# Kernel tuning notes

Measured on AMD Instinct MI355X. Metric: run time of the kernel, lower is better.

## Reference

```python
import jax, jax.numpy as jnp
import numpy as np

B, C, H, W, G = 4, 256, 64, 64, 4
K = 9  # 3x3 kernel


def _conv1x1(x, w, b):
    return jnp.einsum('bchw,oc->bohw', x, w) + b[None, :, None, None]


def _deform_conv(V, offset, mask, weight, groups):
    # torchvision modulated deform_conv2d, stride=1, pad=1, dil=1, no bias.
    Bs, Cc, Hh, Ww = V.shape
    Cg = Cc // groups
    # offset layout: [B, og, K, 2(y,x), H, W]
    off = offset.reshape(Bs, groups, K, 2, Hh, Ww)
    ky, kx = jnp.meshgrid(jnp.arange(3), jnp.arange(3), indexing='ij')
    ky = ky.reshape(K).astype(offset.dtype)
    kx = kx.reshape(K).astype(offset.dtype)
    hh = jnp.arange(Hh, dtype=offset.dtype)
    ww = jnp.arange(Ww, dtype=offset.dtype)
    # sampling positions [B, G, K, H, W]
    py = off[:, :, :, 0] + (hh[:, None] - 1.0)[None, None, None] + ky[None, None, :, None, None]
    px = off[:, :, :, 1] + (ww[None, :] - 1.0)[None, None, None] + kx[None, None, :, None, None]
    y0f = jnp.floor(py)
    x0f = jnp.floor(px)
    fy = py - y0f
    fx = px - x0f
    y0 = y0f.astype(jnp.int32)
    x0 = x0f.astype(jnp.int32)
    Vg = V.reshape(Bs, groups, Cg, Hh * Ww)

    def gather(yi, xi, wgt):
        valid = (yi >= 0) & (yi < Hh) & (xi >= 0) & (xi < Ww)
        idx = (jnp.clip(yi, 0, Hh - 1) * Ww + jnp.clip(xi, 0, Ww - 1)).reshape(Bs, groups, 1, K * Hh * Ww)
        vals = jnp.take_along_axis(Vg, jnp.broadcast_to(idx, (Bs, groups, Cg, K * Hh * Ww)), axis=3)
        vals = vals.reshape(Bs, groups, Cg, K, Hh, Ww)
        return vals * (wgt * valid.astype(wgt.dtype))[:, :, None]

    sampled = (gather(y0, x0, (1.0 - fy) * (1.0 - fx))
               + gather(y0, x0 + 1, (1.0 - fy) * fx)
               + gather(y0 + 1, x0, fy * (1.0 - fx))
               + gather(y0 + 1, x0 + 1, fy * fx))  # [B, G, Cg, K, H, W]
    m = mask.reshape(Bs, groups, K, Hh, Ww)
    wk = weight.reshape(groups, Cc // groups, Cg, K)
    out = jnp.einsum('bgikhw,bgkhw,goik->bgohw', sampled, m, wk)
    return out.reshape(Bs, Cc, Hh, Ww)


def setup_inputs() -> dict:
    key = jax.random.key(0)
    ks = jax.random.split(key, 12)
    inp = {
        'rife_feat': jax.random.normal(ks[0], (B, C, H, W), jnp.float32),
        'd0': jax.random.normal(ks[1], (B, C, H, W), jnp.float32),
        'd1': jax.random.normal(ks[2], (B, C, H, W), jnp.float32),
        'wq': jax.random.normal(ks[3], (C, C), jnp.float32) * (1.0 / np.sqrt(C)),
        'bq': jax.random.normal(ks[4], (C,), jnp.float32) * 0.01,
        'wk': jax.random.normal(ks[5], (C, C), jnp.float32) * (1.0 / np.sqrt(C)),
        'bk': jax.random.normal(ks[6], (C,), jnp.float32) * 0.01,
        'wv': jax.random.normal(ks[7], (C, C), jnp.float32) * (1.0 / np.sqrt(C)),
        'bv': jax.random.normal(ks[8], (C,), jnp.float32) * 0.01,
        'w_off': jax.random.normal(ks[9], (27 * G, 2 * C, 3, 3), jnp.float32) * 0.02,
        'b_off': jnp.zeros((27 * G,), jnp.float32),
        'dcn_w': jax.random.normal(ks[10], (C, C // G, 3, 3), jnp.float32) * 0.05,
        'gamma': jnp.ones((1,), jnp.float32),
    }
    return inp


def reference(rife_feat, d0, d1, wq, bq, wk, bk, wv, bv, w_off, b_off, dcn_w, gamma):
    Qs = jnp.concatenate([rife_feat, rife_feat], axis=0)  # [2B, C, H, W]
    Ds = jnp.concatenate([d0, d1], axis=0)
    Q = _conv1x1(Qs, wq, bq)
    Kf = _conv1x1(Ds, wk, bk)
    V = _conv1x1(Ds, wv, bv)
    comb = jnp.concatenate([Q, Kf], axis=1)  # [2B, 2C, H, W]
    out = jax.lax.conv_general_dilated(comb, w_off, (1, 1), [(1, 1), (1, 1)],
                                       dimension_numbers=('NCHW', 'OIHW', 'NCHW'))
    out = out + b_off[None, :, None, None]  # [2B, 27G, H, W]
    n = out.shape[1] // 3
    o1, o2, mlog = out[:, :n], out[:, n:2 * n], out[:, 2 * n:]
    offset = jnp.concatenate([o1, o2], axis=1)  # [2B, 18G, H, W]
    mask = jax.nn.sigmoid(mlog)
    aligned = _deform_conv(V, offset, mask, dcn_w, G)
    a0, a1 = aligned[:B], aligned[B:]
    fused = rife_feat + gamma * (a0 + a1)
    return fused, offset[:B], offset[B:]
```

## Files before the change

kernel.cpp:

```cpp
#include <hip/hip_runtime.h>
#include <math.h>

#define HW   4096
#define CDIM 256

typedef float f32x4  __attribute__((ext_vector_type(4)));
typedef float f32x2  __attribute__((ext_vector_type(2)));
typedef short short8 __attribute__((ext_vector_type(8)));

#define FUSED_SZ (4ULL*256*HW)
#define OFF_SZ   (4ULL*72*HW)

static __device__ __forceinline__ unsigned short f2b(float f) {
    unsigned u = __float_as_uint(f);
    unsigned r = (u + 0x7fffu + ((u >> 16) & 1u)) >> 16;
    return (unsigned short)r;
}
static __device__ __forceinline__ float b2f(short h) {
    return __uint_as_float(((unsigned)(unsigned short)h) << 16);
}
static __device__ __forceinline__ unsigned pk_bf16(float a, float b) {
    unsigned r;
    asm("v_cvt_pk_bf16_f32 %0, %1, %2" : "=v"(r) : "v"(a), "v"(b));
    return r;
}
union U8 { unsigned u[4]; short8 s; };

#define CVT8(a, HI) ((f32x2)__builtin_amdgcn_cvt_pk_f32_fp8((int)(a), HI))

__global__ __launch_bounds__(256) void prep_all(
    const float* __restrict__ w_off, const float* __restrict__ dcn_w,
    const float* __restrict__ wq, const float* __restrict__ wk,
    const float* __restrict__ wv,
    unsigned short* __restrict__ wT2, unsigned short* __restrict__ dcnwT,
    unsigned short* __restrict__ wqkvT)
{
    const int bid = blockIdx.x;
    if (bid < 2304) {
        int idx = bid * 256 + threadIdx.x;
        int kk  = idx / (128 * 512);
        int rem = idx - kk * 128 * 512;
        int o = rem >> 9;
        int c = rem & 511;
        float v = (o < 108) ? w_off[((size_t)o * 512 + c) * 9 + kk] : 0.f;
        size_t flat = ((size_t)(kk * 16 + (c >> 5)) * 128 + o) * 32 + (c & 31);
        wT2[flat] = f2b(v);
    } else if (bid < 2880) {
        int idx = (bid - 2304) * 256 + threadIdx.x;
        if (idx < 9 * 256 * 64) {
            int k   = idx / (256 * 64);
            int rem = idx - k * 256 * 64;
            int og = rem >> 6;
            int i  = rem & 63;
            int g = og >> 6, ol = og & 63;
            size_t flat = ((size_t)((k * 4 + g) * 2 + (i >> 5)) * 64 + ol) * 32 + (i & 31);
            dcnwT[flat] = f2b(dcn_w[((size_t)og * 64 + i) * 9 + k]);
        }
    } else {
        int idx = (bid - 2880) * 256 + threadIdx.x;
        int o = idx >> 8;
        int c = idx & 255;
        float v = (o < 256) ? wq[(size_t)o * 256 + c]
                : (o < 512) ? wk[(size_t)(o - 256) * 256 + c]
                            : wv[(size_t)(o - 512) * 256 + c];
        wqkvT[idx] = f2b(v);
    }
}

__global__ __launch_bounds__(256) void xprep(
    const float* __restrict__ rife, const float* __restrict__ d0,
    const float* __restrict__ d1, unsigned short* __restrict__ xT)
{
    const int pix0 = blockIdx.x * 64;
    const int img  = blockIdx.y;
    const int t    = threadIdx.x;

    const float* src = (img < 4) ? rife + (size_t)img * CDIM * HW
                     : (img < 8) ? d0 + (size_t)(img - 4) * CDIM * HW
                                 : d1 + (size_t)(img - 8) * CDIM * HW;
    unsigned short* dst = xT + (size_t)img * 4096 * 256;

    __shared__ float tile[64][65];

    for (int c0 = 0; c0 < 256; c0 += 64) {
        #pragma unroll
        for (int r = 0; r < 16; ++r) {
            int idx = t + r * 256;
            int c = idx >> 6, pp = idx & 63;
            tile[c][pp] = src[(size_t)(c0 + c) * HW + pix0 + pp];
        }
        __syncthreads();
        const int pix = t >> 2, cq = t & 3;
        const int cb = cq * 16;
        uint4 p0, p1;
        p0.x = pk_bf16(tile[cb+0][pix],  tile[cb+1][pix]);
        p0.y = pk_bf16(tile[cb+2][pix],  tile[cb+3][pix]);
        p0.z = pk_bf16(tile[cb+4][pix],  tile[cb+5][pix]);
        p0.w = pk_bf16(tile[cb+6][pix],  tile[cb+7][pix]);
        p1.x = pk_bf16(tile[cb+8][pix],  tile[cb+9][pix]);
        p1.y = pk_bf16(tile[cb+10][pix], tile[cb+11][pix]);
        p1.z = pk_bf16(tile[cb+12][pix], tile[cb+13][pix]);
        p1.w = pk_bf16(tile[cb+14][pix], tile[cb+15][pix]);
        unsigned short* p = dst + (size_t)(pix0 + pix) * 256 + c0 + cb;
        *(uint4*)p = p0;
        *(uint4*)(p + 8) = p1;
        __syncthreads();
    }
}

__global__ __launch_bounds__(256) void qkv_mfma(
    const unsigned short* __restrict__ xT,
    const unsigned short* __restrict__ wqkvT,
    const float* __restrict__ bq, const float* __restrict__ bk,
    const float* __restrict__ bv,
    unsigned short* __restrict__ comb_t, unsigned char* __restrict__ vbuf8)
{
    const int pix0 = blockIdx.x * 64;
    const int type = blockIdx.y;
    const int s    = blockIdx.z;
    const int t    = threadIdx.x;
    const int wvi  = t >> 6;
    const int lane = t & 63;
    const int q    = lane >> 4;
    const int rl   = lane & 15;

    const int img = (type == 0) ? (s & 3) : (4 + s);
    const short8* X = (const short8*)(xT + (size_t)img * 4096 * 256);
    const short8* W = (const short8*)(wqkvT + (size_t)(type * 256 + wvi * 64) * 256);
    const float* bias = (type == 0) ? bq : (type == 1) ? bk : bv;

    f32x4 acc[4][4];
    #pragma unroll
    for (int mf = 0; mf < 4; ++mf)
        #pragma unroll
        for (int nf = 0; nf < 4; ++nf)
            acc[mf][nf] = (f32x4){0.f, 0.f, 0.f, 0.f};

    #pragma unroll
    for (int c8 = 0; c8 < 32; c8 += 4) {
        short8 a[4], b[4];
        #pragma unroll
        for (int mf = 0; mf < 4; ++mf)
            a[mf] = W[(size_t)(mf * 16 + rl) * 32 + c8 + q];
        #pragma unroll
        for (int nf = 0; nf < 4; ++nf)
            b[nf] = X[(size_t)(pix0 + nf * 16 + rl) * 32 + c8 + q];
        #pragma unroll
        for (int mf = 0; mf < 4; ++mf)
            #pragma unroll
            for (int nf = 0; nf < 4; ++nf)
                acc[mf][nf] = __builtin_amdgcn_mfma_f32_16x16x32_bf16(a[mf], b[nf], acc[mf][nf], 0, 0, 0);
    }

    if (type < 2) {
        unsigned short* dst = comb_t + (size_t)s * 4096 * 512 + type * 256;
        #pragma unroll
        for (int mf = 0; mf < 4; ++mf) {
            const int o_loc = wvi * 64 + mf * 16 + q * 4;
            const float4 bz = *(const float4*)(bias + o_loc);
            #pragma unroll
            for (int nf = 0; nf < 4; ++nf) {
                const int pix = pix0 + nf * 16 + rl;
                uint2 pk;
                pk.x = pk_bf16(acc[mf][nf][0] + bz.x, acc[mf][nf][1] + bz.y);
                pk.y = pk_bf16(acc[mf][nf][2] + bz.z, acc[mf][nf][3] + bz.w);
                *(uint2*)(dst + (size_t)pix * 512 + o_loc) = pk;
            }
        }
    } else {
        unsigned char* dst8 = vbuf8 + (size_t)s * 4096 * 256;
        #pragma unroll
        for (int mf = 0; mf < 4; ++mf) {
            const int l = mf * 16 + q * 4;
            const int p = wvi * 64 + ((l >> 3) & 3) * 16 + (l >> 5) * 8 + (l & 7);
            const float4 bz = *(const float4*)(bias + wvi * 64 + l);
            #pragma unroll
            for (int nf = 0; nf < 4; ++nf) {
                const int pix = pix0 + nf * 16 + rl;
                int u = __builtin_amdgcn_cvt_pk_fp8_f32(acc[mf][nf][0] + bz.x,
                                                        acc[mf][nf][1] + bz.y, 0, false);
                u = __builtin_amdgcn_cvt_pk_fp8_f32(acc[mf][nf][2] + bz.z,
                                                    acc[mf][nf][3] + bz.w, u, true);
                *(unsigned*)(dst8 + (size_t)pix * 256 + p) = (unsigned)u;
            }
        }
    }
}

__global__ __launch_bounds__(256) void offconv_mfma(
    const unsigned short* __restrict__ comb_t,
    const unsigned short* __restrict__ wT2,
    const float* __restrict__ b_off,
    float* __restrict__ dout, float* __restrict__ mask_ws)
{
    const int bid = blockIdx.x;
    const int s = bid & 7;
    const int h = bid >> 3;
    const int t = threadIdx.x;
    const int lane = t & 63;
    const int wid  = t >> 6;
    const int q    = lane >> 4;
    const int rl   = lane & 15;

    __shared__ __align__(16) unsigned short tb[2][792 * 8];

    const short8* cbv = (const short8*)comb_t + (size_t)s * 4096 * 64;
    const short8* wv  = (const short8*)wT2;

    const int i1 = t + 256, i2 = t + 512, i3 = t + 768;

    auto sload = [&](int idx, int c8) -> short8 {
        int x = idx >> 2, cq = idx & 3;
        int ky = x / 66, xx = x - ky * 66;
        int hh = h + ky - 1, gx = xx - 1;
        short8 v = {0, 0, 0, 0, 0, 0, 0, 0};
        if (hh >= 0 && hh < 64 && gx >= 0 && gx < 64)
            v = cbv[(size_t)(hh * 64 + gx) * 64 + c8 + cq];
        return v;
    };
    auto swrite = [&](unsigned short* buf, int idx, short8 v) {
        int x = idx >> 2, cq = idx & 3;
        int qs = cq ^ ((x >> 1) & 3);
        *((short8*)buf + x * 4 + qs) = v;
    };

    f32x4 acc[2][4];
    #pragma unroll
    for (int ma = 0; ma < 2; ++ma)
        #pragma unroll
        for (int nf = 0; nf < 4; ++nf)
            acc[ma][nf] = (f32x4){0.f, 0.f, 0.f, 0.f};

    short8 r0 = sload(t, 0), r1 = sload(i1, 0), r2 = sload(i2, 0);
    short8 r3 = {0,0,0,0,0,0,0,0};
    if (i3 < 792) r3 = sload(i3, 0);
    swrite(tb[0], t, r0); swrite(tb[0], i1, r1); swrite(tb[0], i2, r2);
    if (i3 < 792) swrite(tb[0], i3, r3);
    __syncthreads();

    for (int sl = 0; sl < 16; ++sl) {
        const int c8 = sl * 4;
        if (sl < 15) {
            r0 = sload(t, c8 + 4); r1 = sload(i1, c8 + 4); r2 = sload(i2, c8 + 4);
            if (i3 < 792) r3 = sload(i3, c8 + 4);
        }
        short8 a[2][9];
        #pragma unroll
        for (int ma = 0; ma < 2; ++ma) {
            const int o = (wid * 2 + ma) * 16 + rl;
            #pragma unroll
            for (int kk = 0; kk < 9; ++kk)
                a[ma][kk] = wv[((size_t)(kk * 16 + sl) * 128 + o) * 4 + q];
        }
        const unsigned short* bufc = tb[sl & 1];
        #pragma unroll
        for (int kk = 0; kk < 9; ++kk) {
            const int ky = kk / 3, kx = kk % 3;
            #pragma unroll
            for (int nf = 0; nf < 4; ++nf) {
                const int xr = ky * 66 + nf * 16 + rl + kx;
                short8 b = *((const short8*)bufc + xr * 4 + (q ^ ((xr >> 1) & 3)));
                acc[0][nf] = __builtin_amdgcn_mfma_f32_16x16x32_bf16(a[0][kk], b, acc[0][nf], 0, 0, 0);
                acc[1][nf] = __builtin_amdgcn_mfma_f32_16x16x32_bf16(a[1][kk], b, acc[1][nf], 0, 0, 0);
            }
        }
        if (sl < 15) {
            unsigned short* bufn = tb[(sl + 1) & 1];
            swrite(bufn, t, r0); swrite(bufn, i1, r1); swrite(bufn, i2, r2);
            if (i3 < 792) swrite(bufn, i3, r3);
        }
        __syncthreads();
    }

    const size_t obase = FUSED_SZ + (s < 4 ? 0 : OFF_SZ) + (size_t)(s & 3) * 72 * HW + (size_t)h * 64;
    const size_t mbase = (size_t)s * 36 * HW + (size_t)h * 64;
    #pragma unroll
    for (int ma = 0; ma < 2; ++ma) {
        #pragma unroll
        for (int r = 0; r < 4; ++r) {
            const int o = (wid * 2 + ma) * 16 + q * 4 + r;
            if (o >= 108) continue;
            const float bz = b_off[o];
            #pragma unroll
            for (int nf = 0; nf < 4; ++nf) {
                const int w = nf * 16 + rl;
                float v = acc[ma][nf][r] + bz;
                if (o < 72)
                    dout[obase + (size_t)o * HW + w] = v;
                else
                    mask_ws[mbase + (size_t)(o - 72) * HW + w] = 1.f / (1.f + expf(-v));
            }
        }
    }
}

__global__ __launch_bounds__(256) void dcn_fuse_mfma(
    const float* __restrict__ rife, const unsigned short* __restrict__ dcnwT,
    const float* __restrict__ gamma,
    const unsigned char* __restrict__ vbuf8, const float* __restrict__ mask_ws,
    float* __restrict__ dout)
{
    const int bid = blockIdx.x;
    const int c   = bid & 15;
    const int h   = bid >> 4;
    const int b   = c >> 2;
    const int g   = c & 3;
    const int t    = threadIdx.x;
    const int wv   = t >> 6;
    const int lane = t & 63;
    const int q    = lane >> 4;
    const int rl   = lane & 15;
    const int pix  = wv * 16 + rl;

    const short8* aT = (const short8*)dcnwT;

    f32x4 acc[4];
    #pragma unroll
    for (int ma = 0; ma < 4; ++ma) acc[ma] = (f32x4){0.f, 0.f, 0.f, 0.f};

    const unsigned obA = (unsigned)(4u * 256u * HW) + (unsigned)((b * 72 + g * 18) * HW + h * 64 + pix);
    const unsigned obB = obA + (unsigned)(4u * 72u * HW);
    const unsigned mbA = (unsigned)((b * 36 + g * 9) * HW + h * 64 + pix);
    const unsigned mbB = mbA + (unsigned)(4u * 36u * HW);
    const unsigned vA  = (unsigned)(b * 4096 * 256 + g * 64 + q * 16);
    const unsigned vB  = vA + 4u * 4096u * 256u;

    auto bil = [&](float py, float px, float mv,
                   float& w00, float& w01, float& w10, float& w11,
                   unsigned& o00, unsigned& o01, unsigned& o10, unsigned& o11) {
        const float y0f = floorf(py), x0f = floorf(px);
        const float fy = py - y0f, fx = px - x0f;
        const int y0 = (int)y0f, x0 = (int)x0f;
        const bool vy0 = (y0 >= 0) && (y0 < 64);
        const bool vy1 = (y0 >= -1) && (y0 < 63);
        const bool vx0 = (x0 >= 0) && (x0 < 64);
        const bool vx1 = (x0 >= -1) && (x0 < 63);
        w00 = (1.f - fy) * (1.f - fx) * mv * (float)(vy0 && vx0);
        w01 = (1.f - fy) * fx        * mv * (float)(vy0 && vx1);
        w10 = fy * (1.f - fx)        * mv * (float)(vy1 && vx0);
        w11 = fy * fx                * mv * (float)(vy1 && vx1);
        const int yc0 = min(max(y0, 0), 63),     yc1 = min(max(y0 + 1, 0), 63);
        const int xc0 = min(max(x0, 0), 63),     xc1 = min(max(x0 + 1, 0), 63);
        o00 = (unsigned)(yc0 * 64 + xc0) * 256u;
        o01 = (unsigned)(yc0 * 64 + xc1) * 256u;
        o10 = (unsigned)(yc1 * 64 + xc0) * 256u;
        o11 = (unsigned)(yc1 * 64 + xc1) * 256u;
    };
    auto blend8 = [&](uint4 c00, uint4 c01, uint4 c10, uint4 c11,
                      float w00, float w01, float w10, float w11,
                      short8& bf0, short8& bf1) {
        U8 u0, u1;
        {
            f32x2 eL = w00*CVT8(c00.x,false) + w01*CVT8(c01.x,false) + w10*CVT8(c10.x,false) + w11*CVT8(c11.x,false);
            f32x2 eH = w00*CVT8(c00.x,true)  + w01*CVT8(c01.x,true)  + w10*CVT8(c10.x,true)  + w11*CVT8(c11.x,true);
            u0.u[0] = pk_bf16(eL.x, eL.y); u0.u[1] = pk_bf16(eH.x, eH.y);
        }
        {
            f32x2 eL = w00*CVT8(c00.y,false) + w01*CVT8(c01.y,false) + w10*CVT8(c10.y,false) + w11*CVT8(c11.y,false);
            f32x2 eH = w00*CVT8(c00.y,true)  + w01*CVT8(c01.y,true)  + w10*CVT8(c10.y,true)  + w11*CVT8(c11.y,true);
            u0.u[2] = pk_bf16(eL.x, eL.y); u0.u[3] = pk_bf16(eH.x, eH.y);
        }
        {
            f32x2 eL = w00*CVT8(c00.z,false) + w01*CVT8(c01.z,false) + w10*CVT8(c10.z,false) + w11*CVT8(c11.z,false);
            f32x2 eH = w00*CVT8(c00.z,true)  + w01*CVT8(c01.z,true)  + w10*CVT8(c10.z,true)  + w11*CVT8(c11.z,true);
            u1.u[0] = pk_bf16(eL.x, eL.y); u1.u[1] = pk_bf16(eH.x, eH.y);
        }
        {
            f32x2 eL = w00*CVT8(c00.w,false) + w01*CVT8(c01.w,false) + w10*CVT8(c10.w,false) + w11*CVT8(c11.w,false);
            f32x2 eH = w00*CVT8(c00.w,true)  + w01*CVT8(c01.w,true)  + w10*CVT8(c10.w,true)  + w11*CVT8(c11.w,true);
            u1.u[2] = pk_bf16(eL.x, eL.y); u1.u[3] = pk_bf16(eH.x, eH.y);
        }
        bf0 = u0.s; bf1 = u1.s;
    };

    float cyA = dout[obA], cxA = dout[obA + (unsigned)HW], cmA = mask_ws[mbA];
    float cyB = dout[obB], cxB = dout[obB + (unsigned)HW], cmB = mask_ws[mbB];

    for (int k = 0; k < 9; ++k) {
        const int ky = k / 3, kx = k - ky * 3;

        float wA00, wA01, wA10, wA11, wB00, wB01, wB10, wB11;
        unsigned oA00, oA01, oA10, oA11, oB00, oB01, oB10, oB11;
        bil(cyA + (float)(h - 1 + ky), cxA + (float)(pix - 1 + kx), cmA,
            wA00, wA01, wA10, wA11, oA00, oA01, oA10, oA11);
        bil(cyB + (float)(h - 1 + ky), cxB + (float)(pix - 1 + kx), cmB,
            wB00, wB01, wB10, wB11, oB00, oB01, oB10, oB11);

        float nyA = cyA, nxA = cxA, nmA = cmA;
        float nyB = cyB, nxB = cxB, nmB = cmB;
        if (k < 8) {
            nyA = dout[obA + (unsigned)((k + 1) * 2 * HW)];
            nxA = dout[obA + (unsigned)(((k + 1) * 2 + 1) * HW)];
            nmA = mask_ws[mbA + (unsigned)((k + 1) * HW)];
            nyB = dout[obB + (unsigned)((k + 1) * 2 * HW)];
            nxB = dout[obB + (unsigned)(((k + 1) * 2 + 1) * HW)];
            nmB = mask_ws[mbB + (unsigned)((k + 1) * HW)];
        }

        short8 af[4][2];
        #pragma unroll
        for (int ma = 0; ma < 4; ++ma)
            #pragma unroll
            for (int ks = 0; ks < 2; ++ks)
                af[ma][ks] = aT[((size_t)((k * 4 + g) * 2 + ks) * 64 + ma * 16 + rl) * 4 + q];

        uint4 A00 = *(const uint4*)(vbuf8 + vA + oA00);
        uint4 A01 = *(const uint4*)(vbuf8 + vA + oA01);
        uint4 A10 = *(const uint4*)(vbuf8 + vA + oA10);
        uint4 A11 = *(const uint4*)(vbuf8 + vA + oA11);
        uint4 B00 = *(const uint4*)(vbuf8 + vB + oB00);
        uint4 B01 = *(const uint4*)(vbuf8 + vB + oB01);
        uint4 B10 = *(const uint4*)(vbuf8 + vB + oB10);
        uint4 B11 = *(const uint4*)(vbuf8 + vB + oB11);

        short8 bf0, bf1;
        blend8(A00, A01, A10, A11, wA00, wA01, wA10, wA11, bf0, bf1);
        acc[0] = __builtin_amdgcn_mfma_f32_16x16x32_bf16(af[0][0], bf0, acc[0], 0, 0, 0);
        acc[1] = __builtin_amdgcn_mfma_f32_16x16x32_bf16(af[1][0], bf0, acc[1], 0, 0, 0);
        acc[2] = __builtin_amdgcn_mfma_f32_16x16x32_bf16(af[2][0], bf0, acc[2], 0, 0, 0);
        acc[3] = __builtin_amdgcn_mfma_f32_16x16x32_bf16(af[3][0], bf0, acc[3], 0, 0, 0);
        acc[0] = __builtin_amdgcn_mfma_f32_16x16x32_bf16(af[0][1], bf1, acc[0], 0, 0, 0);
        acc[1] = __builtin_amdgcn_mfma_f32_16x16x32_bf16(af[1][1], bf1, acc[1], 0, 0, 0);
        acc[2] = __builtin_amdgcn_mfma_f32_16x16x32_bf16(af[2][1], bf1, acc[2], 0, 0, 0);
        acc[3] = __builtin_amdgcn_mfma_f32_16x16x32_bf16(af[3][1], bf1, acc[3], 0, 0, 0);
        blend8(B00, B01, B10, B11, wB00, wB01, wB10, wB11, bf0, bf1);
        acc[0] = __builtin_amdgcn_mfma_f32_16x16x32_bf16(af[0][0], bf0, acc[0], 0, 0, 0);
        acc[1] = __builtin_amdgcn_mfma_f32_16x16x32_bf16(af[1][0], bf0, acc[1], 0, 0, 0);
        acc[2] = __builtin_amdgcn_mfma_f32_16x16x32_bf16(af[2][0], bf0, acc[2], 0, 0, 0);
        acc[3] = __builtin_amdgcn_mfma_f32_16x16x32_bf16(af[3][0], bf0, acc[3], 0, 0, 0);
        acc[0] = __builtin_amdgcn_mfma_f32_16x16x32_bf16(af[0][1], bf1, acc[0], 0, 0, 0);
        acc[1] = __builtin_amdgcn_mfma_f32_16x16x32_bf16(af[1][1], bf1, acc[1], 0, 0, 0);
        acc[2] = __builtin_amdgcn_mfma_f32_16x16x32_bf16(af[2][1], bf1, acc[2], 0, 0, 0);
        acc[3] = __builtin_amdgcn_mfma_f32_16x16x32_bf16(af[3][1], bf1, acc[3], 0, 0, 0);

        cyA = nyA; cxA = nxA; cmA = nmA;
        cyB = nyB; cxB = nxB; cmB = nmB;
    }

    const float gm = gamma[0];
    #pragma unroll
    for (int ma = 0; ma < 4; ++ma) {
        #pragma unroll
        for (int r = 0; r < 4; ++r) {
            const int o = g * 64 + ma * 16 + q * 4 + r;
            const unsigned addr = (unsigned)((b * 256 + o) * HW + h * 64 + pix);
            dout[addr] = rife[addr] + gm * acc[ma][r];
        }
    }
}

extern "C" void kernel_launch(void* const* d_in, const int* in_sizes, int n_in,
                              void* d_out, int out_size, void* d_ws, size_t ws_size,
                              hipStream_t stream)
{
    const float* rife  = (const float*)d_in[0];
    const float* d0    = (const float*)d_in[1];
    const float* d1    = (const float*)d_in[2];
    const float* wq    = (const float*)d_in[3];
    const float* bq    = (const float*)d_in[4];
    const float* wk    = (const float*)d_in[5];
    const float* bk    = (const float*)d_in[6];
    const float* wv    = (const float*)d_in[7];
    const float* bv    = (const float*)d_in[8];
    const float* w_off = (const float*)d_in[9];
    const float* b_off = (const float*)d_in[10];
    const float* dcnw  = (const float*)d_in[11];
    const float* gamma = (const float*)d_in[12];
    float* out = (float*)d_out;
    char* wsb  = (char*)d_ws;

    unsigned short* comb_t = (unsigned short*)(wsb);
    unsigned char*  vbuf8  = (unsigned char*)(wsb + 33554432);
    float*          mws    = (float*)(wsb + 50331648);
    unsigned short* wT2    = (unsigned short*)(wsb + 55050240);
    unsigned short* dcnwT  = (unsigned short*)(wsb + 56229888);
    unsigned short* xT     = (unsigned short*)(wsb + 56524800);
    unsigned short* wqkvT  = (unsigned short*)(wsb + 81690624);

    prep_all<<<3648, 256, 0, stream>>>(w_off, dcnw, wq, wk, wv, wT2, dcnwT, wqkvT);
    xprep<<<dim3(64, 12), 256, 0, stream>>>(rife, d0, d1, xT);
    qkv_mfma<<<dim3(64, 3, 8), 256, 0, stream>>>(xT, wqkvT, bq, bk, bv, comb_t, vbuf8);
    offconv_mfma<<<512, 256, 0, stream>>>(comb_t, wT2, b_off, out, mws);
    dcn_fuse_mfma<<<1024, 256, 0, stream>>>(rife, dcnwT, gamma, vbuf8, mws, out);
}
```

Baseline: 200.1 us.

## Software-pipeline deformable gather loads one tap ahead with double-buffered registers

The 9-tap loop in the deformable-conv MFMA kernel is restructured so the bilinear coordinate computation and the eight 16-byte gathers for tap k+1 are issued before blending and MFMAs consume tap k. Two register sets (even/odd) hold the in-flight gathers, so global load latency can overlap with the matrix work. The cost is higher VGPR pressure, which may lower occupancy, and more code size from the manual unrolling.

```diff
diff --git a/kernel.cpp b/kernel.cpp
--- a/kernel.cpp
+++ b/kernel.cpp
@@ -373,69 +373,77 @@
         bf0 = u0.s; bf1 = u1.s;
     };
 
-    float cyA = dout[obA], cxA = dout[obA + (unsigned)HW], cmA = mask_ws[mbA];
-    float cyB = dout[obB], cxB = dout[obB + (unsigned)HW], cmB = mask_ws[mbB];
-
-    for (int k = 0; k < 9; ++k) {
-        const int ky = k / 3, kx = k - ky * 3;
-
-        float wA00, wA01, wA10, wA11, wB00, wB01, wB10, wB11;
-        unsigned oA00, oA01, oA10, oA11, oB00, oB01, oB10, oB11;
-        bil(cyA + (float)(h - 1 + ky), cxA + (float)(pix - 1 + kx), cmA,
-            wA00, wA01, wA10, wA11, oA00, oA01, oA10, oA11);
-        bil(cyB + (float)(h - 1 + ky), cxB + (float)(pix - 1 + kx), cmB,
-            wB00, wB01, wB10, wB11, oB00, oB01, oB10, oB11);
-
-        float nyA = cyA, nxA = cxA, nmA = cmA;
-        float nyB = cyB, nxB = cxB, nmB = cmB;
-        if (k < 8) {
-            nyA = dout[obA + (unsigned)((k + 1) * 2 * HW)];
-            nxA = dout[obA + (unsigned)(((k + 1) * 2 + 1) * HW)];
-            nmA = mask_ws[mbA + (unsigned)((k + 1) * HW)];
-            nyB = dout[obB + (unsigned)((k + 1) * 2 * HW)];
-            nxB = dout[obB + (unsigned)(((k + 1) * 2 + 1) * HW)];
-            nmB = mask_ws[mbB + (unsigned)((k + 1) * HW)];
-        }
-
-        short8 af[4][2];
-        #pragma unroll
-        for (int ma = 0; ma < 4; ++ma)
-            #pragma unroll
-            for (int ks = 0; ks < 2; ++ks)
-                af[ma][ks] = aT[((size_t)((k * 4 + g) * 2 + ks) * 64 + ma * 16 + rl) * 4 + q];
-
-        uint4 A00 = *(const uint4*)(vbuf8 + vA + oA00);
-        uint4 A01 = *(const uint4*)(vbuf8 + vA + oA01);
-        uint4 A10 = *(const uint4*)(vbuf8 + vA + oA10);
-        uint4 A11 = *(const uint4*)(vbuf8 + vA + oA11);
-        uint4 B00 = *(const uint4*)(vbuf8 + vB + oB00);
-        uint4 B01 = *(const uint4*)(vbuf8 + vB + oB01);
-        uint4 B10 = *(const uint4*)(vbuf8 + vB + oB10);
-        uint4 B11 = *(const uint4*)(vbuf8 + vB + oB11);
-
-        short8 bf0, bf1;
-        blend8(A00, A01, A10, A11, wA00, wA01, wA10, wA11, bf0, bf1);
-        acc[0] = __builtin_amdgcn_mfma_f32_16x16x32_bf16(af[0][0], bf0, acc[0], 0, 0, 0);
-        acc[1] = __builtin_amdgcn_mfma_f32_16x16x32_bf16(af[1][0], bf0, acc[1], 0, 0, 0);
-        acc[2] = __builtin_amdgcn_mfma_f32_16x16x32_bf16(af[2][0], bf0, acc[2], 0, 0, 0);
-        acc[3] = __builtin_amdgcn_mfma_f32_16x16x32_bf16(af[3][0], bf0, acc[3], 0, 0, 0);
-        acc[0] = __builtin_amdgcn_mfma_f32_16x16x32_bf16(af[0][1], bf1, acc[0], 0, 0, 0);
-        acc[1] = __builtin_amdgcn_mfma_f32_16x16x32_bf16(af[1][1], bf1, acc[1], 0, 0, 0);
-        acc[2] = __builtin_amdgcn_mfma_f32_16x16x32_bf16(af[2][1], bf1, acc[2], 0, 0, 0);
-        acc[3] = __builtin_amdgcn_mfma_f32_16x16x32_bf16(af[3][1], bf1, acc[3], 0, 0, 0);
-        blend8(B00, B01, B10, B11, wB00, wB01, wB10, wB11, bf0, bf1);
-        acc[0] = __builtin_amdgcn_mfma_f32_16x16x32_bf16(af[0][0], bf0, acc[0], 0, 0, 0);
-        acc[1] = __builtin_amdgcn_mfma_f32_16x16x32_bf16(af[1][0], bf0, acc[1], 0, 0, 0);
-        acc[2] = __builtin_amdgcn_mfma_f32_16x16x32_bf16(af[2][0], bf0, acc[2], 0, 0, 0);
-        acc[3] = __builtin_amdgcn_mfma_f32_16x16x32_bf16(af[3][0], bf0, acc[3], 0, 0, 0);
-        acc[0] = __builtin_amdgcn_mfma_f32_16x16x32_bf16(af[0][1], bf1, acc[0], 0, 0, 0);
-        acc[1] = __builtin_amdgcn_mfma_f32_16x16x32_bf16(af[1][1], bf1, acc[1], 0, 0, 0);
-        acc[2] = __builtin_amdgcn_mfma_f32_16x16x32_bf16(af[2][1], bf1, acc[2], 0, 0, 0);
-        acc[3] = __builtin_amdgcn_mfma_f32_16x16x32_bf16(af[3][1], bf1, acc[3], 0, 0, 0);
-
-        cyA = nyA; cxA = nxA; cmA = nmA;
-        cyB = nyB; cxB = nxB; cmB = nmB;
-    }
+    float wA00E, wA01E, wA10E, wA11E, wB00E, wB01E, wB10E, wB11E;
+    float wA00O, wA01O, wA10O, wA11O, wB00O, wB01O, wB10O, wB11O;
+    uint4 A00E, A01E, A10E, A11E, B00E, B01E, B10E, B11E;
+    uint4 A00O, A01O, A10O, A11O, B00O, B01O, B10O, B11O;
+
+#define ISSUE(K, S) {                                                          \
+    const int ky_ = (K) / 3, kx_ = (K) - ((K) / 3) * 3;                        \
+    unsigned o0_, o1_, o2_, o3_;                                               \
+    float cy_ = dout[obA + (unsigned)((K) * 2 * HW)];                          \
+    float cx_ = dout[obA + (unsigned)(((K) * 2 + 1) * HW)];                    \
+    float cm_ = mask_ws[mbA + (unsigned)((K) * HW)];                           \
+    bil(cy_ + (float)(h - 1 + ky_), cx_ + (float)(pix - 1 + kx_), cm_,         \
+        wA00##S, wA01##S, wA10##S, wA11##S, o0_, o1_, o2_, o3_);               \
+    A00##S = *(const uint4*)(vbuf8 + vA + o0_);                                \
+    A01##S = *(const uint4*)(vbuf8 + vA + o1_);                                \
+    A10##S = *(const uint4*)(vbuf8 + vA + o2_);                                \
+    A11##S = *(const uint4*)(vbuf8 + vA + o3_);                                \
+    cy_ = dout[obB + (unsigned)((K) * 2 * HW)];                                \
+    cx_ = dout[obB + (unsigned)(((K) * 2 + 1) * HW)];                          \
+    cm_ = mask_ws[mbB + (unsigned)((K) * HW)];                                 \
+    bil(cy_ + (float)(h - 1 + ky_), cx_ + (float)(pix - 1 + kx_), cm_,         \
+        wB00##S, wB01##S, wB10##S, wB11##S, o0_, o1_, o2_, o3_);               \
+    B00##S = *(const uint4*)(vbuf8 + vB + o0_);                                \
+    B01##S = *(const uint4*)(vbuf8 + vB + o1_);                                \
+    B10##S = *(const uint4*)(vbuf8 + vB + o2_);                                \
+    B11##S = *(const uint4*)(vbuf8 + vB + o3_);                                \
+}
+
+#define CONSUME(K, S) {                                                        \
+    short8 af00 = aT[((size_t)((K) * 8 + g * 2 + 0) * 64 + 0 * 16 + rl) * 4 + q]; \
+    short8 af10 = aT[((size_t)((K) * 8 + g * 2 + 0) * 64 + 1 * 16 + rl) * 4 + q]; \
+    short8 af20 = aT[((size_t)((K) * 8 + g * 2 + 0) * 64 + 2 * 16 + rl) * 4 + q]; \
+    short8 af30 = aT[((size_t)((K) * 8 + g * 2 + 0) * 64 + 3 * 16 + rl) * 4 + q]; \
+    short8 af01 = aT[((size_t)((K) * 8 + g * 2 + 1) * 64 + 0 * 16 + rl) * 4 + q]; \
+    short8 af11 = aT[((size_t)((K) * 8 + g * 2 + 1) * 64 + 1 * 16 + rl) * 4 + q]; \
+    short8 af21 = aT[((size_t)((K) * 8 + g * 2 + 1) * 64 + 2 * 16 + rl) * 4 + q]; \
+    short8 af31 = aT[((size_t)((K) * 8 + g * 2 + 1) * 64 + 3 * 16 + rl) * 4 + q]; \
+    short8 bf0_, bf1_;                                                         \
+    blend8(A00##S, A01##S, A10##S, A11##S,                                     \
+           wA00##S, wA01##S, wA10##S, wA11##S, bf0_, bf1_);                    \
+    acc[0] = __builtin_amdgcn_mfma_f32_16x16x32_bf16(af00, bf0_, acc[0], 0, 0, 0); \
+    acc[1] = __builtin_amdgcn_mfma_f32_16x16x32_bf16(af10, bf0_, acc[1], 0, 0, 0); \
+    acc[2] = __builtin_amdgcn_mfma_f32_16x16x32_bf16(af20, bf0_, acc[2], 0, 0, 0); \
+    acc[3] = __builtin_amdgcn_mfma_f32_16x16x32_bf16(af30, bf0_, acc[3], 0, 0, 0); \
+    acc[0] = __builtin_amdgcn_mfma_f32_16x16x32_bf16(af01, bf1_, acc[0], 0, 0, 0); \
+    acc[1] = __builtin_amdgcn_mfma_f32_16x16x32_bf16(af11, bf1_, acc[1], 0, 0, 0); \
+    acc[2] = __builtin_amdgcn_mfma_f32_16x16x32_bf16(af21, bf1_, acc[2], 0, 0, 0); \
+    acc[3] = __builtin_amdgcn_mfma_f32_16x16x32_bf16(af31, bf1_, acc[3], 0, 0, 0); \
+    blend8(B00##S, B01##S, B10##S, B11##S,                                     \
+           wB00##S, wB01##S, wB10##S, wB11##S, bf0_, bf1_);                    \
+    acc[0] = __builtin_amdgcn_mfma_f32_16x16x32_bf16(af00, bf0_, acc[0], 0, 0, 0); \
+    acc[1] = __builtin_amdgcn_mfma_f32_16x16x32_bf16(af10, bf0_, acc[1], 0, 0, 0); \
+    acc[2] = __builtin_amdgcn_mfma_f32_16x16x32_bf16(af20, bf0_, acc[2], 0, 0, 0); \
+    acc[3] = __builtin_amdgcn_mfma_f32_16x16x32_bf16(af30, bf0_, acc[3], 0, 0, 0); \
+    acc[0] = __builtin_amdgcn_mfma_f32_16x16x32_bf16(af01, bf1_, acc[0], 0, 0, 0); \
+    acc[1] = __builtin_amdgcn_mfma_f32_16x16x32_bf16(af11, bf1_, acc[1], 0, 0, 0); \
+    acc[2] = __builtin_amdgcn_mfma_f32_16x16x32_bf16(af21, bf1_, acc[2], 0, 0, 0); \
+    acc[3] = __builtin_amdgcn_mfma_f32_16x16x32_bf16(af31, bf1_, acc[3], 0, 0, 0); \
+}
+
+    ISSUE(0, E);
+    for (int kp = 0; kp < 4; ++kp) {
+        const int k = kp * 2;
+        ISSUE(k + 1, O);
+        CONSUME(k, E);
+        ISSUE(k + 2, E);
+        CONSUME(k + 1, O);
+    }
+    CONSUME(8, E);
+#undef ISSUE
+#undef CONSUME
 
     const float gm = gamma[0];
     #pragma unroll
```

Result: faster. 188.3 us (median of 2 runs) (-5.9%).
